# Kernel tuning notes

Measured on AMD Instinct MI355X. Metric: run time of the kernel, lower is better.

Reference implementation:

```python
import jax, jax.numpy as jnp
import numpy as np

B, V, D, E, F, H, HD = 16, 1024, 16, 64, 16, 128, 64
GRAPH_LAYERS, FLOW_ITERS, DUAL_ITERS = 2, 10, 10
STEP, MOM, BIG = 0.01, 0.9, 1e9


def _build_graph():
    # circulant graph: node v's d-th out-neighbor is v + offs[d] (mod V); offsets paired (o, -o)
    offs = np.array([1, -1, 2, -2, 3, -3, 4, -4, 5, -5, 6, -6, 7, -7, 8, -8], dtype=np.int32)
    v = np.arange(V, dtype=np.int32)[:, None]
    d = np.broadcast_to(np.arange(D, dtype=np.int32)[None, :], (V, D))
    adj = ((v + offs[None, :]) % V).astype(np.int32)
    inv_adj = ((v - offs[None, :]) % V).astype(np.int32)
    in_idx = np.stack([inv_adj, d], axis=-1)    # d-th incoming edge of v == out-edge (inv_adj[v,d], slot d)
    rev_idx = np.stack([adj, d], axis=-1)       # out-edge (v,d) is the d-th incoming edge of adj[v,d]
    opp_idx = np.stack([adj, d ^ 1], axis=-1)   # opposite edge (w->v) is slot d^1 at w (paired offsets)
    bt = lambda x: jnp.asarray(np.broadcast_to(x[None], (B,) + x.shape).copy())
    return bt(adj), bt(inv_adj), bt(in_idx), bt(rev_idx), bt(opp_idx)


def setup_inputs() -> dict:
    key = jax.random.key(0)
    ks = jax.random.split(key, 16)
    adj_lst, inv_adj_lst, in_indices, rev_indices, opp_indices = _build_graph()
    rn = lambda k, shape, scale=1.0: jax.random.normal(k, shape, dtype=jnp.float32) * scale
    s = lambda fan: 1.0 / float(np.sqrt(fan))
    return {
        'demands': rn(ks[0], (B, V, 1)),
        'node_features': rn(ks[1], (B, V, F)),
        'edge_lengths': jax.random.uniform(ks[2], (B, V, D), dtype=jnp.float32),
        'norm_edge_lengths': jax.random.uniform(ks[3], (B, V, D), dtype=jnp.float32),
        'node_emb': rn(ks[4], (V, E)),
        'W_enc': rn(ks[5], (E + F, H), s(E + F)), 'b_enc': jnp.zeros((H,), jnp.float32),
        'W_gat': rn(ks[6], (H, H), s(H)), 'b_gat': jnp.zeros((H,), jnp.float32),
        'a_gat': rn(ks[7], (H,), s(H)),
        'W_gru_x': rn(ks[8], (H, 3 * H), s(H)), 'W_gru_h': rn(ks[9], (H, 3 * H), s(H)),
        'b_gru': jnp.zeros((3 * H,), jnp.float32),
        'W_dec1': rn(ks[10], (2 * H, HD), s(2 * H)), 'b_dec1': jnp.zeros((HD,), jnp.float32),
        'W_dec2': rn(ks[11], (HD, 1), s(HD)), 'b_dec2': jnp.zeros((1,), jnp.float32),
        'W_dual1': rn(ks[12], (H, HD), s(H)), 'b_dual1': jnp.zeros((HD,), jnp.float32),
        'W_dual2': rn(ks[13], (HD, 1), s(HD)), 'b_dual2': jnp.zeros((1,), jnp.float32),
        'adj_lst': adj_lst, 'inv_adj_lst': inv_adj_lst,
        'in_indices': in_indices, 'rev_indices': rev_indices, 'opp_indices': opp_indices,
        'num_nodes': jnp.full((B,), V, dtype=jnp.int32),
    }


def _gather_nodes(values, idx, valid):
    # masked_gather with set_zero=True: values (B,V,H), idx (B,V,D) -> (B,V,D,H)
    bb = jnp.arange(values.shape[0])[:, None, None]
    g = values[bb, jnp.clip(idx, 0, values.shape[1] - 1)]
    return g * valid[..., None]


def _gather_edges(x, idx):
    # gather_nd into a (B,V,D,...) tensor; idx (B,V,D,2) = (node, slot), batch implicit
    bb = jnp.arange(x.shape[0])[:, None, None]
    return x[bb, idx[..., 0], idx[..., 1]]


def _sparsemax(z):
    n = z.shape[-1]
    zs = jnp.sort(z, axis=-1)[..., ::-1]
    k = jnp.arange(1, n + 1, dtype=z.dtype)
    zc = jnp.cumsum(zs, axis=-1)
    support = (1.0 + k * zs) > zc
    kz = jnp.sum(support, axis=-1, keepdims=True)
    tau = (jnp.take_along_axis(zc, kz - 1, axis=-1) - 1.0) / kz.astype(z.dtype)
    return jnp.maximum(z - tau, 0.0)


def _forward(demands, node_features, edge_lengths, norm_edge_lengths, node_emb, W_enc, b_enc,
             W_gat, b_gat, a_gat, W_gru_x, W_gru_h, b_gru, W_dec1, b_dec1, W_dec2, b_dec2,
             W_dual1, b_dual1, W_dual2, b_dual2,
             adj_lst, inv_adj_lst, in_indices, rev_indices, opp_indices, num_nodes):
    f32 = jnp.float32
    # embedding lookup with max_norm=1
    nrm = jnp.linalg.norm(node_emb, axis=-1, keepdims=True)
    emb = node_emb / jnp.maximum(nrm, 1.0)
    emb_b = jnp.broadcast_to(emb[None], (demands.shape[0], V, E))
    node_enc = jnp.concatenate([emb_b, node_features], axis=-1) @ W_enc + b_enc   # (B,V,H)
    mask = (adj_lst == num_nodes[:, None, None]).astype(f32)                       # 1 = padded slot
    valid = 1.0 - mask
    initial = _gather_nodes(node_enc, adj_lst, valid)                              # (B,V,D,H)
    h = initial
    for _ in range(GRAPH_LAYERS):
        # DirectionalGAT: per-edge transform, masked attention over slots, directional regather
        t = jnp.tanh(h @ W_gat + b_gat)                                            # (B,V,D,H)
        logits = jnp.einsum('bvdh,h->bvd', t, a_gat) - BIG * mask
        attn = jax.nn.softmax(logits, axis=-1)
        node_msg = jnp.einsum('bvd,bvdh->bvh', attn, t)                            # (B,V,H)
        msg = _gather_nodes(node_msg, adj_lst, valid)
        x = jnp.tanh(msg + initial)
        # GRU cell, shared weights over all edge states
        gx = x @ W_gru_x + b_gru
        gh = h @ W_gru_h
        z = jax.nn.sigmoid(gx[..., :H] + gh[..., :H])
        r = jax.nn.sigmoid(gx[..., H:2 * H] + gh[..., H:2 * H])
        cand = jnp.tanh(gx[..., 2 * H:] + r * gh[..., 2 * H:])
        h = z * h + (1.0 - z) * cand
    # decoder over (encoding, encoding + opposite-edge encoding)
    comb = h + _gather_edges(h, opp_indices)
    dec_in = jnp.concatenate([h, comb], axis=-1)
    nw = (jnp.tanh(dec_in @ W_dec1 + b_dec1) @ W_dec2 + b_dec2)[..., 0]            # (B,V,D)
    # destination attention: normalize over incoming edges, map back to outgoing layout
    inv_mask = (inv_adj_lst == num_nodes[:, None, None]).astype(f32)
    in_w = _gather_edges(nw, in_indices)
    dest_attn = jax.nn.softmax(in_w - BIG * inv_mask, axis=-1)
    nw = _gather_edges(dest_attn, rev_indices)
    pred = nw - BIG * mask
    normalized = _sparsemax(pred) * valid
    # iterative proportional min-cost-flow solver
    def mcf_step(flow, _):
        inflow = jnp.sum(_gather_edges(flow, in_indices), axis=-1, keepdims=True)  # (B,V,1)
        return normalized * jax.nn.relu(inflow - demands), None
    flow, _ = jax.lax.scan(mcf_step, jnp.zeros_like(normalized), None, length=FLOW_ITERS)
    flow_cost = jnp.sum(flow * flow, axis=(1, 2))                                  # square cost fn
    # dual variables + dual flow (projected momentum gradient descent)
    node_states = jnp.sum(h, axis=2)                                               # (B,V,H)
    dual_vars = jax.nn.relu(jnp.tanh(node_states @ W_dual1 + b_dual1) @ W_dual2 + b_dual2)  # (B,V,1)
    dual = mask * dual_vars
    dual_tr = _gather_nodes(dual_vars, adj_lst, valid)[..., 0]
    dual_diff = dual_tr - dual                                                     # (B,V,D)
    def dual_step(carry, _):
        f, vel = carry
        grad = 2.0 * f + dual_diff                                                 # d/df [f^2 + dual_diff*f]
        vel = MOM * vel - STEP * grad
        f = jax.nn.relu(f + vel)
        return (f, vel), None
    (dual_flows, _), _ = jax.lax.scan(dual_step, (jnp.zeros_like(dual_diff), jnp.zeros_like(dual_diff)), None, length=DUAL_ITERS)
    dual_flows = dual_flows * valid
    dual_demand = jnp.sum(dual_vars * demands, axis=(1, 2))
    dual_cost = jnp.sum(dual_flows * dual_flows + dual_diff * dual_flows, axis=(1, 2)) - dual_demand
    return flow_cost - dual_cost                                                   # (B,) primal-dual gap loss


def reference(demands, node_features, edge_lengths, norm_edge_lengths, node_emb, W_enc, b_enc,
              W_gat, b_gat, a_gat, W_gru_x, W_gru_h, b_gru, W_dec1, b_dec1, W_dec2, b_dec2,
              W_dual1, b_dual1, W_dual2, b_dual2,
              adj_lst, inv_adj_lst, in_indices, rev_indices, opp_indices, num_nodes):
    return _forward(demands, node_features, edge_lengths, norm_edge_lengths, node_emb, W_enc, b_enc,
                    W_gat, b_gat, a_gat, W_gru_x, W_gru_h, b_gru, W_dec1, b_dec1, W_dec2, b_dec2,
                    W_dual1, b_dual1, W_dual2, b_dual2,
                    adj_lst, inv_adj_lst, in_indices, rev_indices, opp_indices, num_nodes)
```

## Files before the change

kernel.cpp:

```cpp
#include <hip/hip_runtime.h>
#include <hip/hip_bf16.h>

#define B 16
#define V 1024
#define D 16
#define E 64
#define F 16
#define H 128
#define HD 64
#define BV (B*V)
#define BVD (B*V*D)

#define OFF_NEBF     0
#define OFF_HNA      (OFF_NEBF + BV*H/2)
#define OFF_HNB      (OFF_HNA + BV*H/2)
#define OFF_NORM     (OFF_HNB + BV*H/2)
#define OFF_DV       (OFF_NORM + BVD)
#define OFF_WT       (OFF_DV + BV)
#define OFF_WTG      (OFF_WT + 65536)
#define OFF_WPQ      (OFF_WTG + 8192)
#define OFF_WU1T     (OFF_WPQ + 8192)

typedef __attribute__((ext_vector_type(8))) short bf16x8;
typedef __attribute__((ext_vector_type(4))) float f32x4;

__device__ __forceinline__ short f2bf(float f){
  __hip_bfloat16 b = __float2bfloat16(f);
  return *reinterpret_cast<short*>(&b);
}
__device__ __forceinline__ float bf2f(short s){
  __hip_bfloat16 b; *reinterpret_cast<short*>(&b) = s;
  return __bfloat162float(b);
}
__device__ __forceinline__ float frcp(float x){ return __builtin_amdgcn_rcpf(x); }
__device__ __forceinline__ float fsig(float x){ return frcp(1.f + __expf(-x)); }
__device__ __forceinline__ float ftanh(float x){
  float e = __expf(-2.f*fabsf(x));
  float r = (1.f - e)*frcp(1.f + e);
  return copysignf(r, x);
}

__global__ __launch_bounds__(256) void k_pre(const float* __restrict__ Wx, const float* __restrict__ Wh,
    const float* __restrict__ Wg, const float* __restrict__ W1, const float* __restrict__ Wu1,
    const float* __restrict__ emb, const float* __restrict__ nf,
    const float* __restrict__ Wenc, const float* __restrict__ benc,
    short* __restrict__ Wt, short* __restrict__ Wgt, short* __restrict__ Wpq,
    short* __restrict__ Wu1t, short* __restrict__ nebf){
  int bid = blockIdx.x, tid = threadIdx.x;
  if (bid < 512){
    int n = bid, k = tid;
    int g = n >> 7, j = n & 127;
    float v;
    if (g == 0)      v = (k < 128) ? Wx[k*384 + j]       : Wh[(k-128)*384 + j];
    else if (g == 1) v = (k < 128) ? Wx[k*384 + 128 + j] : Wh[(k-128)*384 + 128 + j];
    else if (g == 2) v = (k < 128) ? Wx[k*384 + 256 + j] : 0.f;
    else             v = (k < 128) ? 0.f                 : Wh[(k-128)*384 + 256 + j];
    Wt[n*256 + k] = f2bf(v);
    return;
  }
  if (bid < 576){
    int idx = (bid-512)*256 + tid;
    int n = idx >> 7, k = idx & 127;
    Wgt[n*128 + k] = f2bf(Wg[k*128 + n]);
    return;
  }
  if (bid < 608){
    int idx = (bid-576)*256 + tid;
    int n = idx >> 7, k = idx & 127;
    float wb = W1[(k+128)*HD + n];
    float wa = W1[k*HD + n];
    Wpq[n*128 + k]      = f2bf(wa + wb);
    Wpq[(64+n)*128 + k] = f2bf(wb);
    return;
  }
  if (bid < 640){
    int idx = (bid-608)*256 + tid;
    int n = idx >> 7, k = idx & 127;
    Wu1t[n*128 + k] = f2bf(Wu1[k*HD + n]);
    return;
  }
  __shared__ float As[16][80];
  __shared__ float nrmv[16];
  int m0 = (bid - 640)*16;
  {
    int i = tid >> 4, sl = tid & 15;
    int v = (m0 + i) & (V-1);
    float p = 0.f;
    #pragma unroll
    for (int j=0;j<4;j++){ float val = emb[v*E + sl*4 + j]; p += val*val; }
    p += __shfl_down(p, 8);
    p += __shfl_down(p, 4);
    p += __shfl_down(p, 2);
    p += __shfl_down(p, 1);
    if (sl == 0) nrmv[i] = frcp(fmaxf(sqrtf(p), 1.f));
  }
  __syncthreads();
  for (int idx=tid; idx<16*80; idx+=256){
    int i = idx/80, k = idx%80;
    int m = m0 + i; int v = m & (V-1);
    As[i][k] = (k < E) ? emb[v*E + k]*nrmv[i] : nf[m*F + (k-E)];
  }
  __syncthreads();
  int c = tid & 127, half = tid >> 7;
  float acc[8] = {0,0,0,0,0,0,0,0};
  for (int kk=0; kk<80; kk+=4){
    float w[4];
    #pragma unroll
    for (int u=0;u<4;u++) w[u] = Wenc[(kk+u)*H + c];
    #pragma unroll
    for (int i=0;i<8;i++){
      const float4 av = *reinterpret_cast<const float4*>(&As[half*8+i][kk]);
      acc[i] += av.x*w[0] + av.y*w[1] + av.z*w[2] + av.w*w[3];
    }
  }
  float bb = benc[c];
  #pragma unroll
  for (int i=0;i<8;i++){
    int m = m0 + half*8 + i;
    nebf[m*H + c] = f2bf(acc[i] + bb);
  }
}

__global__ __launch_bounds__(256) void k_layer(const short* __restrict__ hin, const short* __restrict__ nebf,
    const int* __restrict__ adj, const short* __restrict__ Wgt, const float* __restrict__ bg,
    const float* __restrict__ ag, const short* __restrict__ Wt, const float* __restrict__ bgru,
    short* __restrict__ hout){
  __shared__ short Hs[80][136];
  __shared__ short Ts[80][136];
  __shared__ short Xs[64][136];
  __shared__ float Lp[4][80];
  __shared__ float Ls[80];
  int tid = threadIdx.x;
  int blk = blockIdx.x;
  int b = blk >> 4;
  int n0 = (blk & 15) << 6;
  for (int idx=tid; idx<80*16; idx+=256){
    int r = idx >> 4, c8 = idx & 15;
    int g = (b << 10) + ((n0 - 8 + r) & 1023);
    *reinterpret_cast<bf16x8*>(&Hs[r][c8*8]) =
        *reinterpret_cast<const bf16x8*>(&hin[(long)g*128 + c8*8]);
  }
  __syncthreads();
  int w = tid >> 6, lane = tid & 63;
  int l15 = lane & 15, quad = lane >> 4;
  {
    f32x4 acc[5][2];
    #pragma unroll
    for (int mt=0;mt<5;mt++)
      #pragma unroll
      for (int u=0;u<2;u++) acc[mt][u] = (f32x4){0.f,0.f,0.f,0.f};
    #pragma unroll
    for (int kc=0;kc<4;kc++){
      int k0 = kc*32;
      bf16x8 a[5];
      #pragma unroll
      for (int mt=0;mt<5;mt++)
        a[mt] = *reinterpret_cast<const bf16x8*>(&Hs[16*mt + l15][k0 + quad*8]);
      #pragma unroll
      for (int u=0;u<2;u++){
        bf16x8 bfr = *reinterpret_cast<const bf16x8*>(&Wgt[(32*w + 16*u + l15)*128 + k0 + quad*8]);
        #pragma unroll
        for (int mt=0;mt<5;mt++)
          acc[mt][u] = __builtin_amdgcn_mfma_f32_16x16x32_bf16(a[mt], bfr, acc[mt][u], 0,0,0);
      }
    }
    float lp[5][4];
    #pragma unroll
    for (int mt=0;mt<5;mt++)
      #pragma unroll
      for (int reg=0;reg<4;reg++) lp[mt][reg] = 0.f;
    #pragma unroll
    for (int u=0;u<2;u++){
      int c = 32*w + 16*u + l15;
      float bgc = bg[c], agc = ag[c];
      #pragma unroll
      for (int mt=0;mt<5;mt++){
        #pragma unroll
        for (int reg=0;reg<4;reg++){
          float t = ftanh(acc[mt][u][reg] + bgc);
          Ts[16*mt + quad*4 + reg][c] = f2bf(t);
          lp[mt][reg] += t * agc;
        }
      }
    }
    #pragma unroll
    for (int mt=0;mt<5;mt++)
      #pragma unroll
      for (int reg=0;reg<4;reg++){
        lp[mt][reg] += __shfl_xor(lp[mt][reg], 1);
        lp[mt][reg] += __shfl_xor(lp[mt][reg], 2);
        lp[mt][reg] += __shfl_xor(lp[mt][reg], 4);
        lp[mt][reg] += __shfl_xor(lp[mt][reg], 8);
      }
    if (l15 == 0){
      #pragma unroll
      for (int mt=0;mt<5;mt++)
        #pragma unroll
        for (int reg=0;reg<4;reg++)
          Lp[w][16*mt + quad*4 + reg] = lp[mt][reg];
    }
  }
  __syncthreads();
  if (tid < 80) Ls[tid] = Lp[0][tid]+Lp[1][tid]+Lp[2][tid]+Lp[3][tid];
  __syncthreads();
  {
    int vl = tid >> 2, seg = tid & 3;
    int vg = (b<<10) + n0 + vl;
    int li[16]; float at[16];
    float m = -1e30f;
    #pragma unroll
    for (int d=0; d<16; d++){
      int a = adj[vg*16 + d];
      li[d] = (a - n0 + 8) & 1023;
      m = fmaxf(m, Ls[li[d]]);
    }
    float s = 0.f;
    #pragma unroll
    for (int d=0; d<16; d++){ at[d] = __expf(Ls[li[d]] - m); s += at[d]; }
    float inv = frcp(s);
    #pragma unroll
    for (int d=0; d<16; d++) at[d] *= inv;
    #pragma unroll
    for (int c8=0; c8<4; c8++){
      int c = seg*32 + c8*8;
      float acc8[8] = {0,0,0,0,0,0,0,0};
      #pragma unroll 4
      for (int d=0; d<16; d++){
        bf16x8 tv = *reinterpret_cast<const bf16x8*>(&Ts[li[d]][c]);
        float a = at[d];
        #pragma unroll
        for (int q=0;q<8;q++) acc8[q] += a * bf2f(tv[q]);
      }
      bf16x8 nv = *reinterpret_cast<const bf16x8*>(&nebf[(long)vg*128 + c]);
      bf16x8 xv;
      #pragma unroll
      for (int q=0;q<8;q++) xv[q] = f2bf(ftanh(acc8[q] + bf2f(nv[q])));
      *reinterpret_cast<bf16x8*>(&Xs[vl][c]) = xv;
    }
  }
  __syncthreads();
  f32x4 acc[4][4][2];
  #pragma unroll
  for (int mt=0;mt<4;mt++)
    #pragma unroll
    for (int g=0;g<4;g++)
      #pragma unroll
      for (int u=0;u<2;u++) acc[mt][g][u] = (f32x4){0.f,0.f,0.f,0.f};
  for (int k8=0;k8<8;k8++){
    int k0 = k8*32;
    int gg = (k8 < 4) ? 2 : 3;
    bf16x8 a[4];
    #pragma unroll
    for (int mt=0;mt<4;mt++){
      if (k8 < 4) a[mt] = *reinterpret_cast<const bf16x8*>(&Xs[16*mt + l15][k0 + quad*8]);
      else        a[mt] = *reinterpret_cast<const bf16x8*>(&Hs[16*mt + l15 + 8][k0 - 128 + quad*8]);
    }
    bf16x8 bz[2], br[2], bc[2];
    #pragma unroll
    for (int u=0;u<2;u++){
      int ncol = 32*w + 16*u + l15;
      int koff = k0 + quad*8;
      bz[u] = *reinterpret_cast<const bf16x8*>(&Wt[(ncol      )*256 + koff]);
      br[u] = *reinterpret_cast<const bf16x8*>(&Wt[(ncol + 128)*256 + koff]);
      bc[u] = *reinterpret_cast<const bf16x8*>(&Wt[(ncol + gg*128)*256 + koff]);
    }
    #pragma unroll
    for (int mt=0;mt<4;mt++){
      #pragma unroll
      for (int u=0;u<2;u++){
        acc[mt][0][u]  = __builtin_amdgcn_mfma_f32_16x16x32_bf16(a[mt], bz[u], acc[mt][0][u], 0,0,0);
        acc[mt][1][u]  = __builtin_amdgcn_mfma_f32_16x16x32_bf16(a[mt], br[u], acc[mt][1][u], 0,0,0);
        acc[mt][gg][u] = __builtin_amdgcn_mfma_f32_16x16x32_bf16(a[mt], bc[u], acc[mt][gg][u], 0,0,0);
      }
    }
  }
  __syncthreads();
  #pragma unroll
  for (int u=0;u<2;u++){
    int j = 32*w + 16*u + l15;
    float bjz = bgru[j], bjr = bgru[128 + j], bjc = bgru[256 + j];
    #pragma unroll
    for (int mt=0;mt<4;mt++){
      #pragma unroll
      for (int reg=0;reg<4;reg++){
        int rl = 16*mt + quad*4 + reg;
        float z = fsig(acc[mt][0][u][reg] + bjz);
        float r = fsig(acc[mt][1][u][reg] + bjr);
        float cand = ftanh(acc[mt][2][u][reg] + bjc + r*acc[mt][3][u][reg]);
        float ho = bf2f(Hs[rl + 8][j]);
        Xs[rl][j] = f2bf(z*ho + (1.f - z)*cand);
      }
    }
  }
  __syncthreads();
  for (int idx=tid; idx<64*16; idx+=256){
    int r = idx >> 4, c8 = idx & 15;
    *reinterpret_cast<bf16x8*>(&hout[(long)((b<<10) + n0 + r)*128 + c8*8]) =
        *reinterpret_cast<const bf16x8*>(&Xs[r][c8*8]);
  }
}

__global__ __launch_bounds__(256) void k_decdas(const short* __restrict__ hn, const int* __restrict__ adj,
    const int* __restrict__ invadj, const short* __restrict__ Wpq, const float* __restrict__ b1,
    const float* __restrict__ W2, const float* __restrict__ b2_,
    const short* __restrict__ Wu1t, const float* __restrict__ bu1, const float* __restrict__ Wu2,
    const float* __restrict__ bu2_, float* __restrict__ norm_, float* __restrict__ dv){
  __shared__ short Hs[112][136];
  __shared__ short PQb[112][132];
  __shared__ short NSs[64][136];
  __shared__ int adjL[64][16];
  __shared__ float dvp[64][4];
  __shared__ float b1s[64], w2s[64], bu1s[64], wu2s[64];
  int tid = threadIdx.x;
  int blk = blockIdx.x;
  int b = blk >> 4;
  int n0 = (blk & 15) << 6;
  if (tid < 64){ b1s[tid] = b1[tid]; w2s[tid] = W2[tid]; bu1s[tid] = bu1[tid]; wu2s[tid] = Wu2[tid]; }
  for (int idx=tid; idx<112*16; idx+=256){
    int r = idx >> 4, c8 = idx & 15;
    int g = (b << 10) + ((n0 - 24 + r) & 1023);
    *reinterpret_cast<bf16x8*>(&Hs[r][c8*8]) =
        *reinterpret_cast<const bf16x8*>(&hn[(long)g*128 + c8*8]);
  }
  #pragma unroll
  for (int e=0;e<4;e++){
    int idx = e*256 + tid;
    int r = idx >> 4, d = idx & 15;
    int a = adj[((b<<10) + n0 + r)*16 + d];
    adjL[r][d] = (a - n0 + 24) & 1023;
  }
  __syncthreads();
  int w = tid >> 6, lane = tid & 63;
  int l15 = lane & 15, quad = lane >> 4;
  {
    f32x4 acc[7][2];
    #pragma unroll
    for (int mt=0;mt<7;mt++)
      #pragma unroll
      for (int u=0;u<2;u++) acc[mt][u] = (f32x4){0.f,0.f,0.f,0.f};
    #pragma unroll
    for (int kc=0;kc<4;kc++){
      int k0 = kc*32;
      bf16x8 a[7];
      #pragma unroll
      for (int mt=0;mt<7;mt++)
        a[mt] = *reinterpret_cast<const bf16x8*>(&Hs[16*mt + l15][k0 + quad*8]);
      #pragma unroll
      for (int u=0;u<2;u++){
        bf16x8 bfr = *reinterpret_cast<const bf16x8*>(&Wpq[(32*w + 16*u + l15)*128 + k0 + quad*8]);
        #pragma unroll
        for (int mt=0;mt<7;mt++)
          acc[mt][u] = __builtin_amdgcn_mfma_f32_16x16x32_bf16(a[mt], bfr, acc[mt][u], 0,0,0);
      }
    }
    #pragma unroll
    for (int u=0;u<2;u++){
      int c = 32*w + 16*u + l15;
      #pragma unroll
      for (int mt=0;mt<7;mt++)
        #pragma unroll
        for (int reg=0;reg<4;reg++)
          PQb[16*mt + quad*4 + reg][c] = f2bf(acc[mt][u][reg]);
    }
  }
  #pragma unroll
  for (int e=0;e<4;e++){
    int idx = e*256 + tid;
    int r = idx >> 4, c8 = idx & 15;
    float acc8[8] = {0,0,0,0,0,0,0,0};
    #pragma unroll 4
    for (int d=0; d<16; d++){
      bf16x8 hv = *reinterpret_cast<const bf16x8*>(&Hs[adjL[r][d]][c8*8]);
      #pragma unroll
      for (int q=0;q<8;q++) acc8[q] += bf2f(hv[q]);
    }
    bf16x8 sv;
    #pragma unroll
    for (int q=0;q<8;q++) sv[q] = f2bf(acc8[q]);
    *reinterpret_cast<bf16x8*>(&NSs[r][c8*8]) = sv;
  }
  __syncthreads();
  {
    f32x4 acc[4];
    #pragma unroll
    for (int mt=0;mt<4;mt++) acc[mt] = (f32x4){0.f,0.f,0.f,0.f};
    #pragma unroll
    for (int kc=0;kc<4;kc++){
      int k0 = kc*32;
      bf16x8 bfr = *reinterpret_cast<const bf16x8*>(&Wu1t[(16*w + l15)*128 + k0 + quad*8]);
      #pragma unroll
      for (int mt=0;mt<4;mt++){
        bf16x8 a = *reinterpret_cast<const bf16x8*>(&NSs[16*mt + l15][k0 + quad*8]);
        acc[mt] = __builtin_amdgcn_mfma_f32_16x16x32_bf16(a, bfr, acc[mt], 0,0,0);
      }
    }
    int n = 16*w + l15;
    float bn = bu1s[n], wn = wu2s[n];
    #pragma unroll
    for (int mt=0;mt<4;mt++){
      #pragma unroll
      for (int reg=0;reg<4;reg++){
        float p = ftanh(acc[mt][reg] + bn) * wn;
        p += __shfl_xor(p, 1);
        p += __shfl_xor(p, 2);
        p += __shfl_xor(p, 4);
        p += __shfl_xor(p, 8);
        if (l15 == 0) dvp[16*mt + quad*4 + reg][w] = p;
      }
    }
  }
  __syncthreads();
  float* nws = reinterpret_cast<float*>(&Hs[0][0]);
  float b2v = b2_[0];
  for (int e = tid; e < 96*16; e += 256){
    int rr = e >> 4, d = e & 15;
    int wnode = (n0 + rr - 16) & 1023;
    int wg = (b<<10) + wnode;
    int a = adj[wg*16 + d];
    int al = (a - n0 + 24) & 1023;
    int wl = rr + 8;
    float p = 0.f;
    #pragma unroll 8
    for (int c=0;c<64;c++)
      p += ftanh(bf2f(PQb[al][c]) + bf2f(PQb[wl][64 + c]) + b1s[c]) * w2s[c];
    nws[rr*17 + d] = p + b2v;
  }
  __syncthreads();
  if (tid < 64){
    float val = dvp[tid][0]+dvp[tid][1]+dvp[tid][2]+dvp[tid][3];
    dv[(b<<10) + n0 + tid] = fmaxf(val + bu2_[0], 0.f);
  }
  float* datt = reinterpret_cast<float*>(&PQb[0][0]);
  if (tid < 80){
    int wnode = (n0 + tid - 8) & 1023;
    int wg = (b<<10) + wnode;
    float vals[16];
    float m = -1e30f;
    #pragma unroll
    for (int d=0; d<16; d++){
      int iv = invadj[wg*16 + d];
      int il = (iv - n0 + 16) & 1023;
      vals[d] = nws[il*17 + d];
      m = fmaxf(m, vals[d]);
    }
    float s = 0.f;
    #pragma unroll
    for (int d=0; d<16; d++){ vals[d] = __expf(vals[d]-m); s += vals[d]; }
    float inv = frcp(s);
    #pragma unroll
    for (int d=0; d<16; d++) datt[tid*17 + d] = vals[d]*inv;
  }
  __syncthreads();
  if (tid < 64){
    int vg = (b<<10) + n0 + tid;
    float z[16], s[16];
    #pragma unroll
    for (int d=0; d<16; d++){
      int al = adjL[tid][d] - 16;
      z[d] = datt[al*17 + d];
      s[d] = z[d];
    }
    #pragma unroll
    for (int k2 = 2; k2 <= 16; k2 <<= 1){
      #pragma unroll
      for (int jj = k2 >> 1; jj > 0; jj >>= 1){
        #pragma unroll
        for (int i = 0; i < 16; i++){
          int l = i ^ jj;
          if (l > i){
            bool up = ((i & k2) == 0);
            float a = s[i], bb = s[l];
            bool sw = up ? (a > bb) : (a < bb);
            if (sw){ s[i]=bb; s[l]=a; }
          }
        }
      }
    }
    float cs = 0.f, zcs = 0.f; int kz = 1;
    #pragma unroll
    for (int j=0;j<16;j++){
      float zj = s[15-j];
      cs += zj;
      if (1.f + (float)(j+1)*zj > cs){ kz = j+1; zcs = cs; }
    }
    float tau = (zcs - 1.f)/(float)kz;
    #pragma unroll
    for (int d=0; d<16; d++) norm_[(long)vg*16 + d] = fmaxf(z[d]-tau, 0.f);
  }
}

__global__ __launch_bounds__(1024) void k_flowfin(const float* __restrict__ norm_,
    const float* __restrict__ dem, const int* __restrict__ invadj, const float* __restrict__ dv,
    float* __restrict__ out){
  __shared__ float nrmS[V*17];
  __shared__ float sbuf[2][V];
  __shared__ float r1[16], r2[16], r3[16];
  int b = blockIdx.x, v = threadIdx.x;
  int gv = (b<<10) + v;
  {
    const float4* src = reinterpret_cast<const float4*>(&norm_[(long)gv*16]);
    #pragma unroll
    for (int q4=0; q4<4; q4++){
      float4 x = src[q4];
      nrmS[v*17 + q4*4+0] = x.x; nrmS[v*17 + q4*4+1] = x.y;
      nrmS[v*17 + q4*4+2] = x.z; nrmS[v*17 + q4*4+3] = x.w;
    }
  }
  int iv[16];
  #pragma unroll
  for (int d4=0; d4<4; d4++){
    int4 i4 = reinterpret_cast<const int4*>(&invadj[(long)gv*16])[d4];
    iv[d4*4+0]=i4.x; iv[d4*4+1]=i4.y; iv[d4*4+2]=i4.z; iv[d4*4+3]=i4.w;
  }
  float dm = dem[gv];
  sbuf[0][v] = 0.f;
  __syncthreads();
  float nrg[16]; float nr2 = 0.f;
  #pragma unroll
  for (int d=0; d<16; d++){
    nrg[d] = nrmS[iv[d]*17 + d];
    float nv = nrmS[v*17 + d];
    nr2 += nv*nv;
  }
  int p = 0;
  float s = 0.f;
  for (int it=0; it<10; it++){
    float inflow = 0.f;
    #pragma unroll
    for (int d=0; d<16; d++) inflow += nrg[d]*sbuf[p][iv[d]];
    s = fmaxf(inflow - dm, 0.f);
    sbuf[1-p][v] = s;
    p ^= 1;
    __syncthreads();
  }
  float partF = nr2 * s * s;
  float dvv = dv[gv];
  float f = 0.f, vel = 0.f;
  #pragma unroll
  for (int it=0; it<10; it++){
    float g = 2.f*f + dvv;
    vel = 0.9f*vel - 0.01f*g;
    f = fmaxf(f + vel, 0.f);
  }
  float partD = f*f + dvv*f;
  float partDD = dvv * dm;
  #pragma unroll
  for (int off=32; off>0; off>>=1){
    partF  += __shfl_down(partF, off);
    partD  += __shfl_down(partD, off);
    partDD += __shfl_down(partDD, off);
  }
  if ((v & 63) == 0){ r1[v>>6] = partF; r2[v>>6] = partD; r3[v>>6] = partDD; }
  __syncthreads();
  if (v == 0){
    float sf = 0.f, sd = 0.f, sdd = 0.f;
    #pragma unroll
    for (int i=0;i<16;i++){ sf += r1[i]; sd += r2[i]; sdd += r3[i]; }
    out[b] = sf - (16.f*sd - sdd);
  }
}

extern "C" void kernel_launch(void* const* d_in, const int* in_sizes, int n_in,
                              void* d_out, int out_size, void* d_ws, size_t ws_size,
                              hipStream_t stream){
  (void)in_sizes; (void)n_in; (void)out_size; (void)ws_size;
  const float* demands = (const float*)d_in[0];
  const float* nf      = (const float*)d_in[1];
  const float* emb     = (const float*)d_in[4];
  const float* Wenc    = (const float*)d_in[5];
  const float* benc    = (const float*)d_in[6];
  const float* Wgat    = (const float*)d_in[7];
  const float* bgat    = (const float*)d_in[8];
  const float* agat    = (const float*)d_in[9];
  const float* Wgx     = (const float*)d_in[10];
  const float* Wgh     = (const float*)d_in[11];
  const float* bgru    = (const float*)d_in[12];
  const float* Wd1     = (const float*)d_in[13];
  const float* bd1     = (const float*)d_in[14];
  const float* Wd2     = (const float*)d_in[15];
  const float* bd2     = (const float*)d_in[16];
  const float* Wu1     = (const float*)d_in[17];
  const float* bu1     = (const float*)d_in[18];
  const float* Wu2     = (const float*)d_in[19];
  const float* bu2     = (const float*)d_in[20];
  const int* adj       = (const int*)d_in[21];
  const int* invadj    = (const int*)d_in[22];

  float* ws    = (float*)d_ws;
  short* nebf  = (short*)(ws + OFF_NEBF);
  short* hnA   = (short*)(ws + OFF_HNA);
  short* hnB   = (short*)(ws + OFF_HNB);
  float* nrm   = ws + OFF_NORM;
  float* dv    = ws + OFF_DV;
  short* wt    = (short*)(ws + OFF_WT);
  short* wtg   = (short*)(ws + OFF_WTG);
  short* wpq   = (short*)(ws + OFF_WPQ);
  short* wu1t  = (short*)(ws + OFF_WU1T);

  k_pre<<<1664, 256, 0, stream>>>(Wgx, Wgh, Wgat, Wd1, Wu1, emb, nf, Wenc, benc,
                                  wt, wtg, wpq, wu1t, nebf);
  k_layer<<<BV/64, 256, 0, stream>>>(nebf, nebf, adj, wtg, bgat, agat, wt, bgru, hnA);
  k_layer<<<BV/64, 256, 0, stream>>>(hnA, nebf, adj, wtg, bgat, agat, wt, bgru, hnB);
  k_decdas<<<BV/64, 256, 0, stream>>>(hnB, adj, invadj, wpq, bd1, Wd2, bd2,
                                      wu1t, bu1, Wu2, bu2, nrm, dv);
  k_flowfin<<<B, 1024, 0, stream>>>(nrm, demands, invadj, dv, (float*)d_out);
}
```

Baseline: 205.7 us.

## Fuse encoder and both GAT-GRU layers into one kernel with halo recompute

Merges the node encoder and the two graph layers into a single kernel. Each block recomputes a wider halo (96 rows for layer one, 80 for layer two) so the intermediate embeddings and first-layer hidden states stay in shared memory rather than going through global memory. The encoder is also moved onto bf16 MFMA using a transposed, zero-padded weight matrix built in k_pre. The trade-off is extra redundant halo computation, more shared memory per block (likely lower occupancy), and one fewer launch plus one fewer grid-wide dependency.

```diff
diff --git a/kernel.cpp b/kernel.cpp
--- a/kernel.cpp
+++ b/kernel.cpp
@@ -11,15 +11,14 @@
 #define BV (B*V)
 #define BVD (B*V*D)
 
-#define OFF_NEBF     0
-#define OFF_HNA      (OFF_NEBF + BV*H/2)
-#define OFF_HNB      (OFF_HNA + BV*H/2)
+#define OFF_HNB      0
 #define OFF_NORM     (OFF_HNB + BV*H/2)
 #define OFF_DV       (OFF_NORM + BVD)
 #define OFF_WT       (OFF_DV + BV)
 #define OFF_WTG      (OFF_WT + 65536)
 #define OFF_WPQ      (OFF_WTG + 8192)
 #define OFF_WU1T     (OFF_WPQ + 8192)
+#define OFF_WENCT    (OFF_WU1T + 4096)
 
 typedef __attribute__((ext_vector_type(8))) short bf16x8;
 typedef __attribute__((ext_vector_type(4))) float f32x4;
@@ -42,10 +41,9 @@
 
 __global__ __launch_bounds__(256) void k_pre(const float* __restrict__ Wx, const float* __restrict__ Wh,
     const float* __restrict__ Wg, const float* __restrict__ W1, const float* __restrict__ Wu1,
-    const float* __restrict__ emb, const float* __restrict__ nf,
-    const float* __restrict__ Wenc, const float* __restrict__ benc,
+    const float* __restrict__ Wenc,
     short* __restrict__ Wt, short* __restrict__ Wgt, short* __restrict__ Wpq,
-    short* __restrict__ Wu1t, short* __restrict__ nebf){
+    short* __restrict__ Wu1t, short* __restrict__ Wenct){
   int bid = blockIdx.x, tid = threadIdx.x;
   if (bid < 512){
     int n = bid, k = tid;
@@ -79,94 +77,117 @@
     Wu1t[n*128 + k] = f2bf(Wu1[k*HD + n]);
     return;
   }
-  __shared__ float As[16][80];
-  __shared__ float nrmv[16];
-  int m0 = (bid - 640)*16;
-  {
-    int i = tid >> 4, sl = tid & 15;
-    int v = (m0 + i) & (V-1);
-    float p = 0.f;
-    #pragma unroll
-    for (int j=0;j<4;j++){ float val = emb[v*E + sl*4 + j]; p += val*val; }
-    p += __shfl_down(p, 8);
-    p += __shfl_down(p, 4);
-    p += __shfl_down(p, 2);
-    p += __shfl_down(p, 1);
-    if (sl == 0) nrmv[i] = frcp(fmaxf(sqrtf(p), 1.f));
-  }
-  __syncthreads();
-  for (int idx=tid; idx<16*80; idx+=256){
-    int i = idx/80, k = idx%80;
-    int m = m0 + i; int v = m & (V-1);
-    As[i][k] = (k < E) ? emb[v*E + k]*nrmv[i] : nf[m*F + (k-E)];
-  }
-  __syncthreads();
-  int c = tid & 127, half = tid >> 7;
-  float acc[8] = {0,0,0,0,0,0,0,0};
-  for (int kk=0; kk<80; kk+=4){
-    float w[4];
-    #pragma unroll
-    for (int u=0;u<4;u++) w[u] = Wenc[(kk+u)*H + c];
-    #pragma unroll
-    for (int i=0;i<8;i++){
-      const float4 av = *reinterpret_cast<const float4*>(&As[half*8+i][kk]);
-      acc[i] += av.x*w[0] + av.y*w[1] + av.z*w[2] + av.w*w[3];
-    }
-  }
-  float bb = benc[c];
-  #pragma unroll
-  for (int i=0;i<8;i++){
-    int m = m0 + half*8 + i;
-    nebf[m*H + c] = f2bf(acc[i] + bb);
+  {
+    int nn = (bid-640)*2 + (tid >> 7);
+    int kk = tid & 127;
+    if (kk < 96) Wenct[nn*96 + kk] = f2bf(kk < 80 ? Wenc[kk*128 + nn] : 0.f);
   }
 }
 
-__global__ __launch_bounds__(256) void k_layer(const short* __restrict__ hin, const short* __restrict__ nebf,
-    const int* __restrict__ adj, const short* __restrict__ Wgt, const float* __restrict__ bg,
-    const float* __restrict__ ag, const short* __restrict__ Wt, const float* __restrict__ bgru,
-    short* __restrict__ hout){
-  __shared__ short Hs[80][136];
-  __shared__ short Ts[80][136];
-  __shared__ short Xs[64][136];
-  __shared__ float Lp[4][80];
-  __shared__ float Ls[80];
+__global__ __launch_bounds__(256) void k_mega(const float* __restrict__ emb, const float* __restrict__ nf,
+    const short* __restrict__ Wenct, const float* __restrict__ benc, const int* __restrict__ adj,
+    const short* __restrict__ Wgt, const float* __restrict__ bg, const float* __restrict__ ag,
+    const short* __restrict__ Wt, const float* __restrict__ bgru, short* __restrict__ hout){
+  __shared__ short NE[96][136];
+  __shared__ short T[96][136];
+  __shared__ short H1[80][136];
+  __shared__ short X[80][136];
+  __shared__ float Lp[4][96];
+  __shared__ float Ls[96];
+  __shared__ float nrmv[96];
+  short (*As)[104] = reinterpret_cast<short(*)[104]>(&H1[0][0]);
+
   int tid = threadIdx.x;
   int blk = blockIdx.x;
   int b = blk >> 4;
   int n0 = (blk & 15) << 6;
-  for (int idx=tid; idx<80*16; idx+=256){
-    int r = idx >> 4, c8 = idx & 15;
-    int g = (b << 10) + ((n0 - 8 + r) & 1023);
-    *reinterpret_cast<bf16x8*>(&Hs[r][c8*8]) =
-        *reinterpret_cast<const bf16x8*>(&hin[(long)g*128 + c8*8]);
-  }
-  __syncthreads();
   int w = tid >> 6, lane = tid & 63;
   int l15 = lane & 15, quad = lane >> 4;
-  {
-    f32x4 acc[5][2];
-    #pragma unroll
-    for (int mt=0;mt<5;mt++)
+
+  if (tid < 96){
+    int v = (n0 - 16 + tid) & 1023;
+    const float4* e4 = reinterpret_cast<const float4*>(&emb[v*E]);
+    float ss = 0.f;
+    #pragma unroll
+    for (int q=0;q<16;q++){ float4 x = e4[q]; ss += x.x*x.x + x.y*x.y + x.z*x.z + x.w*x.w; }
+    nrmv[tid] = frcp(fmaxf(sqrtf(ss), 1.f));
+  }
+  __syncthreads();
+  for (int e=tid; e<96*16; e+=256){
+    int r = e >> 4, q = e & 15;
+    int v = (n0 - 16 + r) & 1023;
+    float4 x = reinterpret_cast<const float4*>(&emb[v*E])[q];
+    float iv = nrmv[r];
+    short4 s; s.x=f2bf(x.x*iv); s.y=f2bf(x.y*iv); s.z=f2bf(x.z*iv); s.w=f2bf(x.w*iv);
+    *reinterpret_cast<short4*>(&As[r][q*4]) = s;
+  }
+  for (int e=tid; e<96*4; e+=256){
+    int r = e >> 2, q = e & 3;
+    int m = (b<<10) + ((n0 - 16 + r) & 1023);
+    float4 x = reinterpret_cast<const float4*>(&nf[(long)m*F])[q];
+    short4 s; s.x=f2bf(x.x); s.y=f2bf(x.y); s.z=f2bf(x.z); s.w=f2bf(x.w);
+    *reinterpret_cast<short4*>(&As[r][64 + q*4]) = s;
+    short4 z; z.x=0; z.y=0; z.z=0; z.w=0;
+    *reinterpret_cast<short4*>(&As[r][80 + q*4]) = z;
+  }
+  __syncthreads();
+  {
+    f32x4 acc[6][2];
+    #pragma unroll
+    for (int mt=0;mt<6;mt++)
+      #pragma unroll
+      for (int u=0;u<2;u++) acc[mt][u] = (f32x4){0.f,0.f,0.f,0.f};
+    #pragma unroll
+    for (int kc=0;kc<3;kc++){
+      int k0 = kc*32;
+      bf16x8 a[6];
+      #pragma unroll
+      for (int mt=0;mt<6;mt++)
+        a[mt] = *reinterpret_cast<const bf16x8*>(&As[16*mt + l15][k0 + quad*8]);
+      #pragma unroll
+      for (int u=0;u<2;u++){
+        bf16x8 bfr = *reinterpret_cast<const bf16x8*>(&Wenct[(32*w + 16*u + l15)*96 + k0 + quad*8]);
+        #pragma unroll
+        for (int mt=0;mt<6;mt++)
+          acc[mt][u] = __builtin_amdgcn_mfma_f32_16x16x32_bf16(a[mt], bfr, acc[mt][u], 0,0,0);
+      }
+    }
+    #pragma unroll
+    for (int u=0;u<2;u++){
+      int c = 32*w + 16*u + l15;
+      float bb = benc[c];
+      #pragma unroll
+      for (int mt=0;mt<6;mt++)
+        #pragma unroll
+        for (int reg=0;reg<4;reg++)
+          NE[16*mt + quad*4 + reg][c] = f2bf(acc[mt][u][reg] + bb);
+    }
+  }
+  __syncthreads();
+  {
+    f32x4 acc[6][2];
+    #pragma unroll
+    for (int mt=0;mt<6;mt++)
       #pragma unroll
       for (int u=0;u<2;u++) acc[mt][u] = (f32x4){0.f,0.f,0.f,0.f};
     #pragma unroll
     for (int kc=0;kc<4;kc++){
       int k0 = kc*32;
-      bf16x8 a[5];
-      #pragma unroll
-      for (int mt=0;mt<5;mt++)
-        a[mt] = *reinterpret_cast<const bf16x8*>(&Hs[16*mt + l15][k0 + quad*8]);
+      bf16x8 a[6];
+      #pragma unroll
+      for (int mt=0;mt<6;mt++)
+        a[mt] = *reinterpret_cast<const bf16x8*>(&NE[16*mt + l15][k0 + quad*8]);
       #pragma unroll
       for (int u=0;u<2;u++){
         bf16x8 bfr = *reinterpret_cast<const bf16x8*>(&Wgt[(32*w + 16*u + l15)*128 + k0 + quad*8]);
         #pragma unroll
-        for (int mt=0;mt<5;mt++)
+        for (int mt=0;mt<6;mt++)
           acc[mt][u] = __builtin_amdgcn_mfma_f32_16x16x32_bf16(a[mt], bfr, acc[mt][u], 0,0,0);
       }
     }
-    float lp[5][4];
-    #pragma unroll
-    for (int mt=0;mt<5;mt++)
+    float lp[6][4];
+    #pragma unroll
+    for (int mt=0;mt<6;mt++)
       #pragma unroll
       for (int reg=0;reg<4;reg++) lp[mt][reg] = 0.f;
     #pragma unroll
@@ -174,17 +195,17 @@
       int c = 32*w + 16*u + l15;
       float bgc = bg[c], agc = ag[c];
       #pragma unroll
-      for (int mt=0;mt<5;mt++){
+      for (int mt=0;mt<6;mt++){
         #pragma unroll
         for (int reg=0;reg<4;reg++){
           float t = ftanh(acc[mt][u][reg] + bgc);
-          Ts[16*mt + quad*4 + reg][c] = f2bf(t);
+          T[16*mt + quad*4 + reg][c] = f2bf(t);
           lp[mt][reg] += t * agc;
         }
       }
     }
     #pragma unroll
-    for (int mt=0;mt<5;mt++)
+    for (int mt=0;mt<6;mt++)
       #pragma unroll
       for (int reg=0;reg<4;reg++){
         lp[mt][reg] += __shfl_xor(lp[mt][reg], 1);
@@ -194,24 +215,24 @@
       }
     if (l15 == 0){
       #pragma unroll
-      for (int mt=0;mt<5;mt++)
+      for (int mt=0;mt<6;mt++)
         #pragma unroll
         for (int reg=0;reg<4;reg++)
           Lp[w][16*mt + quad*4 + reg] = lp[mt][reg];
     }
   }
   __syncthreads();
-  if (tid < 80) Ls[tid] = Lp[0][tid]+Lp[1][tid]+Lp[2][tid]+Lp[3][tid];
-  __syncthreads();
-  {
-    int vl = tid >> 2, seg = tid & 3;
-    int vg = (b<<10) + n0 + vl;
+  if (tid < 96) Ls[tid] = Lp[0][tid]+Lp[1][tid]+Lp[2][tid]+Lp[3][tid];
+  __syncthreads();
+  for (int e=tid; e<320; e+=256){
+    int vl = e >> 2, seg = e & 3;
+    int wg = (b<<10) + ((n0 - 8 + vl) & 1023);
     int li[16]; float at[16];
     float m = -1e30f;
     #pragma unroll
     for (int d=0; d<16; d++){
-      int a = adj[vg*16 + d];
-      li[d] = (a - n0 + 8) & 1023;
+      int a = adj[wg*16 + d];
+      li[d] = (a - n0 + 16) & 1023;
       m = fmaxf(m, Ls[li[d]]);
     }
     float s = 0.f;
@@ -226,69 +247,222 @@
       float acc8[8] = {0,0,0,0,0,0,0,0};
       #pragma unroll 4
       for (int d=0; d<16; d++){
-        bf16x8 tv = *reinterpret_cast<const bf16x8*>(&Ts[li[d]][c]);
+        bf16x8 tv = *reinterpret_cast<const bf16x8*>(&T[li[d]][c]);
         float a = at[d];
         #pragma unroll
         for (int q=0;q<8;q++) acc8[q] += a * bf2f(tv[q]);
       }
-      bf16x8 nv = *reinterpret_cast<const bf16x8*>(&nebf[(long)vg*128 + c]);
+      bf16x8 nv = *reinterpret_cast<const bf16x8*>(&NE[vl + 8][c]);
       bf16x8 xv;
       #pragma unroll
       for (int q=0;q<8;q++) xv[q] = f2bf(ftanh(acc8[q] + bf2f(nv[q])));
-      *reinterpret_cast<bf16x8*>(&Xs[vl][c]) = xv;
-    }
-  }
-  __syncthreads();
-  f32x4 acc[4][4][2];
-  #pragma unroll
-  for (int mt=0;mt<4;mt++)
-    #pragma unroll
-    for (int g=0;g<4;g++)
-      #pragma unroll
-      for (int u=0;u<2;u++) acc[mt][g][u] = (f32x4){0.f,0.f,0.f,0.f};
-  for (int k8=0;k8<8;k8++){
-    int k0 = k8*32;
-    int gg = (k8 < 4) ? 2 : 3;
-    bf16x8 a[4];
-    #pragma unroll
-    for (int mt=0;mt<4;mt++){
-      if (k8 < 4) a[mt] = *reinterpret_cast<const bf16x8*>(&Xs[16*mt + l15][k0 + quad*8]);
-      else        a[mt] = *reinterpret_cast<const bf16x8*>(&Hs[16*mt + l15 + 8][k0 - 128 + quad*8]);
-    }
-    bf16x8 bz[2], br[2], bc[2];
+      *reinterpret_cast<bf16x8*>(&X[vl][c]) = xv;
+    }
+  }
+  __syncthreads();
+  {
+    f32x4 acc[5][4][2];
+    #pragma unroll
+    for (int mt=0;mt<5;mt++)
+      #pragma unroll
+      for (int g=0;g<4;g++)
+        #pragma unroll
+        for (int u=0;u<2;u++) acc[mt][g][u] = (f32x4){0.f,0.f,0.f,0.f};
+    for (int k8=0;k8<8;k8++){
+      int k0 = k8*32;
+      int gg = (k8 < 4) ? 2 : 3;
+      bf16x8 a[5];
+      #pragma unroll
+      for (int mt=0;mt<5;mt++){
+        if (k8 < 4) a[mt] = *reinterpret_cast<const bf16x8*>(&X[16*mt + l15][k0 + quad*8]);
+        else        a[mt] = *reinterpret_cast<const bf16x8*>(&NE[16*mt + l15 + 8][k0 - 128 + quad*8]);
+      }
+      bf16x8 bz[2], br[2], bc[2];
+      #pragma unroll
+      for (int u=0;u<2;u++){
+        int ncol = 32*w + 16*u + l15;
+        int koff = k0 + quad*8;
+        bz[u] = *reinterpret_cast<const bf16x8*>(&Wt[(ncol      )*256 + koff]);
+        br[u] = *reinterpret_cast<const bf16x8*>(&Wt[(ncol + 128)*256 + koff]);
+        bc[u] = *reinterpret_cast<const bf16x8*>(&Wt[(ncol + gg*128)*256 + koff]);
+      }
+      #pragma unroll
+      for (int mt=0;mt<5;mt++){
+        #pragma unroll
+        for (int u=0;u<2;u++){
+          acc[mt][0][u]  = __builtin_amdgcn_mfma_f32_16x16x32_bf16(a[mt], bz[u], acc[mt][0][u], 0,0,0);
+          acc[mt][1][u]  = __builtin_amdgcn_mfma_f32_16x16x32_bf16(a[mt], br[u], acc[mt][1][u], 0,0,0);
+          acc[mt][gg][u] = __builtin_amdgcn_mfma_f32_16x16x32_bf16(a[mt], bc[u], acc[mt][gg][u], 0,0,0);
+        }
+      }
+    }
     #pragma unroll
     for (int u=0;u<2;u++){
-      int ncol = 32*w + 16*u + l15;
-      int koff = k0 + quad*8;
-      bz[u] = *reinterpret_cast<const bf16x8*>(&Wt[(ncol      )*256 + koff]);
-      br[u] = *reinterpret_cast<const bf16x8*>(&Wt[(ncol + 128)*256 + koff]);
-      bc[u] = *reinterpret_cast<const bf16x8*>(&Wt[(ncol + gg*128)*256 + koff]);
-    }
-    #pragma unroll
-    for (int mt=0;mt<4;mt++){
+      int j = 32*w + 16*u + l15;
+      float bjz = bgru[j], bjr = bgru[128 + j], bjc = bgru[256 + j];
+      #pragma unroll
+      for (int mt=0;mt<5;mt++){
+        #pragma unroll
+        for (int reg=0;reg<4;reg++){
+          int rl = 16*mt + quad*4 + reg;
+          float z = fsig(acc[mt][0][u][reg] + bjz);
+          float r = fsig(acc[mt][1][u][reg] + bjr);
+          float cand = ftanh(acc[mt][2][u][reg] + bjc + r*acc[mt][3][u][reg]);
+          float ho = bf2f(NE[rl + 8][j]);
+          H1[rl][j] = f2bf(z*ho + (1.f - z)*cand);
+        }
+      }
+    }
+  }
+  __syncthreads();
+  {
+    f32x4 acc[5][2];
+    #pragma unroll
+    for (int mt=0;mt<5;mt++)
+      #pragma unroll
+      for (int u=0;u<2;u++) acc[mt][u] = (f32x4){0.f,0.f,0.f,0.f};
+    #pragma unroll
+    for (int kc=0;kc<4;kc++){
+      int k0 = kc*32;
+      bf16x8 a[5];
+      #pragma unroll
+      for (int mt=0;mt<5;mt++)
+        a[mt] = *reinterpret_cast<const bf16x8*>(&H1[16*mt + l15][k0 + quad*8]);
       #pragma unroll
       for (int u=0;u<2;u++){
-        acc[mt][0][u]  = __builtin_amdgcn_mfma_f32_16x16x32_bf16(a[mt], bz[u], acc[mt][0][u], 0,0,0);
-        acc[mt][1][u]  = __builtin_amdgcn_mfma_f32_16x16x32_bf16(a[mt], br[u], acc[mt][1][u], 0,0,0);
-        acc[mt][gg][u] = __builtin_amdgcn_mfma_f32_16x16x32_bf16(a[mt], bc[u], acc[mt][gg][u], 0,0,0);
-      }
-    }
-  }
-  __syncthreads();
-  #pragma unroll
-  for (int u=0;u<2;u++){
-    int j = 32*w + 16*u + l15;
-    float bjz = bgru[j], bjr = bgru[128 + j], bjc = bgru[256 + j];
-    #pragma unroll
-    for (int mt=0;mt<4;mt++){
+        bf16x8 bfr = *reinterpret_cast<const bf16x8*>(&Wgt[(32*w + 16*u + l15)*128 + k0 + quad*8]);
+        #pragma unroll
+        for (int mt=0;mt<5;mt++)
+          acc[mt][u] = __builtin_amdgcn_mfma_f32_16x16x32_bf16(a[mt], bfr, acc[mt][u], 0,0,0);
+      }
+    }
+    float lp[5][4];
+    #pragma unroll
+    for (int mt=0;mt<5;mt++)
+      #pragma unroll
+      for (int reg=0;reg<4;reg++) lp[mt][reg] = 0.f;
+    #pragma unroll
+    for (int u=0;u<2;u++){
+      int c = 32*w + 16*u + l15;
+      float bgc = bg[c], agc = ag[c];
+      #pragma unroll
+      for (int mt=0;mt<5;mt++){
+        #pragma unroll
+        for (int reg=0;reg<4;reg++){
+          float t = ftanh(acc[mt][u][reg] + bgc);
+          T[16*mt + quad*4 + reg][c] = f2bf(t);
+          lp[mt][reg] += t * agc;
+        }
+      }
+    }
+    #pragma unroll
+    for (int mt=0;mt<5;mt++)
       #pragma unroll
       for (int reg=0;reg<4;reg++){
-        int rl = 16*mt + quad*4 + reg;
-        float z = fsig(acc[mt][0][u][reg] + bjz);
-        float r = fsig(acc[mt][1][u][reg] + bjr);
-        float cand = ftanh(acc[mt][2][u][reg] + bjc + r*acc[mt][3][u][reg]);
-        float ho = bf2f(Hs[rl + 8][j]);
-        Xs[rl][j] = f2bf(z*ho + (1.f - z)*cand);
+        lp[mt][reg] += __shfl_xor(lp[mt][reg], 1);
+        lp[mt][reg] += __shfl_xor(lp[mt][reg], 2);
+        lp[mt][reg] += __shfl_xor(lp[mt][reg], 4);
+        lp[mt][reg] += __shfl_xor(lp[mt][reg], 8);
+      }
+    if (l15 == 0){
+      #pragma unroll
+      for (int mt=0;mt<5;mt++)
+        #pragma unroll
+        for (int reg=0;reg<4;reg++)
+          Lp[w][16*mt + quad*4 + reg] = lp[mt][reg];
+    }
+  }
+  __syncthreads();
+  if (tid < 80) Ls[tid] = Lp[0][tid]+Lp[1][tid]+Lp[2][tid]+Lp[3][tid];
+  __syncthreads();
+  {
+    int vl = tid >> 2, seg = tid & 3;
+    int vg = (b<<10) + n0 + vl;
+    int li[16]; float at[16];
+    float m = -1e30f;
+    #pragma unroll
+    for (int d=0; d<16; d++){
+      int a = adj[vg*16 + d];
+      li[d] = (a - n0 + 8) & 1023;
+      m = fmaxf(m, Ls[li[d]]);
+    }
+    float s = 0.f;
+    #pragma unroll
+    for (int d=0; d<16; d++){ at[d] = __expf(Ls[li[d]] - m); s += at[d]; }
+    float inv = frcp(s);
+    #pragma unroll
+    for (int d=0; d<16; d++) at[d] *= inv;
+    #pragma unroll
+    for (int c8=0; c8<4; c8++){
+      int c = seg*32 + c8*8;
+      float acc8[8] = {0,0,0,0,0,0,0,0};
+      #pragma unroll 4
+      for (int d=0; d<16; d++){
+        bf16x8 tv = *reinterpret_cast<const bf16x8*>(&T[li[d]][c]);
+        float a = at[d];
+        #pragma unroll
+        for (int q=0;q<8;q++) acc8[q] += a * bf2f(tv[q]);
+      }
+      bf16x8 nv = *reinterpret_cast<const bf16x8*>(&NE[vl + 16][c]);
+      bf16x8 xv;
+      #pragma unroll
+      for (int q=0;q<8;q++) xv[q] = f2bf(ftanh(acc8[q] + bf2f(nv[q])));
+      *reinterpret_cast<bf16x8*>(&X[vl][c]) = xv;
+    }
+  }
+  __syncthreads();
+  {
+    f32x4 acc[4][4][2];
+    #pragma unroll
+    for (int mt=0;mt<4;mt++)
+      #pragma unroll
+      for (int g=0;g<4;g++)
+        #pragma unroll
+        for (int u=0;u<2;u++) acc[mt][g][u] = (f32x4){0.f,0.f,0.f,0.f};
+    for (int k8=0;k8<8;k8++){
+      int k0 = k8*32;
+      int gg = (k8 < 4) ? 2 : 3;
+      bf16x8 a[4];
+      #pragma unroll
+      for (int mt=0;mt<4;mt++){
+        if (k8 < 4) a[mt] = *reinterpret_cast<const bf16x8*>(&X[16*mt + l15][k0 + quad*8]);
+        else        a[mt] = *reinterpret_cast<const bf16x8*>(&H1[16*mt + l15 + 8][k0 - 128 + quad*8]);
+      }
+      bf16x8 bz[2], br[2], bc[2];
+      #pragma unroll
+      for (int u=0;u<2;u++){
+        int ncol = 32*w + 16*u + l15;
+        int koff = k0 + quad*8;
+        bz[u] = *reinterpret_cast<const bf16x8*>(&Wt[(ncol      )*256 + koff]);
+        br[u] = *reinterpret_cast<const bf16x8*>(&Wt[(ncol + 128)*256 + koff]);
+        bc[u] = *reinterpret_cast<const bf16x8*>(&Wt[(ncol + gg*128)*256 + koff]);
+      }
+      #pragma unroll
+      for (int mt=0;mt<4;mt++){
+        #pragma unroll
+        for (int u=0;u<2;u++){
+          acc[mt][0][u]  = __builtin_amdgcn_mfma_f32_16x16x32_bf16(a[mt], bz[u], acc[mt][0][u], 0,0,0);
+          acc[mt][1][u]  = __builtin_amdgcn_mfma_f32_16x16x32_bf16(a[mt], br[u], acc[mt][1][u], 0,0,0);
+          acc[mt][gg][u] = __builtin_amdgcn_mfma_f32_16x16x32_bf16(a[mt], bc[u], acc[mt][gg][u], 0,0,0);
+        }
+      }
+    }
+    __syncthreads();
+    #pragma unroll
+    for (int u=0;u<2;u++){
+      int j = 32*w + 16*u + l15;
+      float bjz = bgru[j], bjr = bgru[128 + j], bjc = bgru[256 + j];
+      #pragma unroll
+      for (int mt=0;mt<4;mt++){
+        #pragma unroll
+        for (int reg=0;reg<4;reg++){
+          int rl = 16*mt + quad*4 + reg;
+          float z = fsig(acc[mt][0][u][reg] + bjz);
+          float r = fsig(acc[mt][1][u][reg] + bjr);
+          float cand = ftanh(acc[mt][2][u][reg] + bjc + r*acc[mt][3][u][reg]);
+          float ho = bf2f(H1[rl + 8][j]);
+          X[rl][j] = f2bf(z*ho + (1.f - z)*cand);
+        }
       }
     }
   }
@@ -296,7 +470,7 @@
   for (int idx=tid; idx<64*16; idx+=256){
     int r = idx >> 4, c8 = idx & 15;
     *reinterpret_cast<bf16x8*>(&hout[(long)((b<<10) + n0 + r)*128 + c8*8]) =
-        *reinterpret_cast<const bf16x8*>(&Xs[r][c8*8]);
+        *reinterpret_cast<const bf16x8*>(&X[r][c8*8]);
   }
 }
 
@@ -587,8 +761,6 @@
   const int* invadj    = (const int*)d_in[22];
 
   float* ws    = (float*)d_ws;
-  short* nebf  = (short*)(ws + OFF_NEBF);
-  short* hnA   = (short*)(ws + OFF_HNA);
   short* hnB   = (short*)(ws + OFF_HNB);
   float* nrm   = ws + OFF_NORM;
   float* dv    = ws + OFF_DV;
@@ -596,11 +768,10 @@
   short* wtg   = (short*)(ws + OFF_WTG);
   short* wpq   = (short*)(ws + OFF_WPQ);
   short* wu1t  = (short*)(ws + OFF_WU1T);
-
-  k_pre<<<1664, 256, 0, stream>>>(Wgx, Wgh, Wgat, Wd1, Wu1, emb, nf, Wenc, benc,
-                                  wt, wtg, wpq, wu1t, nebf);
-  k_layer<<<BV/64, 256, 0, stream>>>(nebf, nebf, adj, wtg, bgat, agat, wt, bgru, hnA);
-  k_layer<<<BV/64, 256, 0, stream>>>(hnA, nebf, adj, wtg, bgat, agat, wt, bgru, hnB);
+  short* wenct = (short*)(ws + OFF_WENCT);
+
+  k_pre<<<704, 256, 0, stream>>>(Wgx, Wgh, Wgat, Wd1, Wu1, Wenc, wt, wtg, wpq, wu1t, wenct);
+  k_mega<<<BV/64, 256, 0, stream>>>(emb, nf, wenct, benc, adj, wtg, bgat, agat, wt, bgru, hnB);
   k_decdas<<<BV/64, 256, 0, stream>>>(hnB, adj, invadj, wpq, bd1, Wd2, bd2,
                                       wu1t, bu1, Wu2, bu2, nrm, dv);
   k_flowfin<<<B, 1024, 0, stream>>>(nrm, demands, invadj, dv, (float*)d_out);
```

Result: no change. 201.9 us (-1.9%).
